# Performance work log

Hardware: AMD Instinct MI355X
Metric: run time of the kernel (lower is better)

## Reference

```python
import jax, jax.numpy as jnp
import numpy as np

BETA = 0.1
MARGIN = 0.1
LOSS_WEIGHT = 1.0
K = 4          # num_negative_samples_per_positive
EPS = 1e-6
C, D, P = 100000, 256, 65536


def _energy(p, c):
    """Euclidean entailment-cone energy: relu(apex_angle(p,c) - aperture(p))."""
    diff = c - p
    num = jnp.sum(c * c, -1) - jnp.sum(p * p, -1) - jnp.sum(diff * diff, -1)
    norm_p = jnp.linalg.norm(p, axis=-1)
    denom = 2.0 * norm_p * jnp.linalg.norm(diff, axis=-1) + EPS
    cosang = jnp.clip(num / denom, -1.0 + EPS, 1.0 - EPS)
    ang = jnp.arccos(cosang)
    aperture = jnp.arcsin(jnp.clip(BETA / (norm_p + EPS), 0.0, 1.0 - EPS))
    return jax.nn.relu(ang - aperture)


def setup_inputs() -> dict:
    key = jax.random.key(0)
    k1, k2, k3 = jax.random.split(key, 3)
    prototypes = jax.random.normal(k1, (C, D), dtype=jnp.float32)
    pairs = jax.random.randint(k2, (P, 2), 0, C, dtype=jnp.int32)
    neg_c = jax.random.randint(k3, (P * K,), 0, C, dtype=jnp.int32)
    return {"prototypes": prototypes, "pairs": pairs, "neg_c": neg_c}


def reference(prototypes, pairs, neg_c):
    # positive pairs: (parent, child) gathers
    p_pos = prototypes[pairs[:, 0]]                    # [P, D]
    c_pos = prototypes[pairs[:, 1]]                    # [P, D]
    avg_pos = _energy(p_pos, c_pos).mean()

    # negatives: each positive parent repeated K times vs sampled neg children
    neg_p_idx = jnp.repeat(pairs[:, 0], K)             # [P*K]
    p_neg = prototypes[neg_p_idx]                      # [P*K, D]
    c_neg = prototypes[neg_c]                          # [P*K, D]
    avg_neg = jax.nn.relu(MARGIN - _energy(p_neg, c_neg)).mean()

    return (avg_pos + avg_neg) * 0.5 * LOSS_WEIGHT
```

## Files before the change

kernel.cpp:

```cpp
#include <hip/hip_runtime.h>

#define BETA   0.1f
#define MARGIN 0.1f
#define EPSF   1e-6f
#define KNEG   4

__device__ __forceinline__ float gsum16(float v) {
    #pragma unroll
    for (int off = 8; off >= 1; off >>= 1)
        v += __shfl_xor(v, off, 64);
    return v;
}

__device__ __forceinline__ float wave_sum(float v) {
    #pragma unroll
    for (int off = 32; off >= 1; off >>= 1)
        v += __shfl_xor(v, off, 64);
    return v;
}

__device__ __forceinline__ float dot4(float4 a, float4 b) {
    return a.x*b.x + a.y*b.y + a.z*b.z + a.w*b.w;
}

__global__ __launch_bounds__(256) void cone_main(
    const float* __restrict__ proto,
    const int*   __restrict__ pairs,
    const int*   __restrict__ negc,
    float*       __restrict__ part,
    int P)
{
    const int lane = threadIdx.x & 63;
    const int wid  = threadIdx.x >> 6;
    const int sub  = lane >> 4;
    const int sl   = lane & 15;
    const int pair = (blockIdx.x * 4 + wid) * 4 + sub;

    float pos_e = 0.f, neg_e = 0.f;
    if (pair < P) {
        const int pi = pairs[2 * pair];
        int idx[5];
        idx[0] = pairs[2 * pair + 1];
        #pragma unroll
        for (int k = 0; k < KNEG; ++k) idx[1 + k] = negc[4 * pair + k];

        const float4* prow = (const float4*)(proto + (size_t)pi * 256);
        float4 pv[4];
        #pragma unroll
        for (int r = 0; r < 4; ++r) pv[r] = prow[sl + 16 * r];

        float4 cv[5][4];
        #pragma unroll
        for (int j = 0; j < 5; ++j) {
            const float4* crow = (const float4*)(proto + (size_t)idx[j] * 256);
            #pragma unroll
            for (int r = 0; r < 4; ++r) cv[j][r] = crow[sl + 16 * r];
        }

        float pp = 0.f;
        #pragma unroll
        for (int r = 0; r < 4; ++r) pp += dot4(pv[r], pv[r]);
        float p2     = gsum16(pp);
        float norm_p = sqrtf(p2);
        float apert  = asinf(fminf(fmaxf(BETA / (norm_p + EPSF), 0.f), 1.f - EPSF));

        #pragma unroll
        for (int j = 0; j < 5; ++j) {
            float cc = 0.f, dd = 0.f;
            #pragma unroll
            for (int r = 0; r < 4; ++r) {
                float4 c = cv[j][r], p = pv[r];
                cc += dot4(c, c);
                float dx = c.x - p.x, dy = c.y - p.y, dz = c.z - p.z, dw = c.w - p.w;
                dd += dx*dx + dy*dy + dz*dz + dw*dw;
            }
            float c2 = gsum16(cc);
            float d2 = gsum16(dd);
            float num    = c2 - p2 - d2;
            float denom  = 2.f * norm_p * sqrtf(d2) + EPSF;
            float cosang = fminf(fmaxf(num / denom, -1.f + EPSF), 1.f - EPSF);
            float e      = fmaxf(acosf(cosang) - apert, 0.f);
            if (j == 0) pos_e = e;
            else        neg_e += fmaxf(MARGIN - e, 0.f);
        }
    }

    __shared__ float sp[16], sn[16];
    if (sl == 0) { sp[wid * 4 + sub] = pos_e; sn[wid * 4 + sub] = neg_e; }
    __syncthreads();
    if (threadIdx.x == 0) {
        float ps = 0.f, ns = 0.f;
        #pragma unroll
        for (int i = 0; i < 16; ++i) { ps += sp[i]; ns += sn[i]; }
        part[2 * blockIdx.x]     = ps;
        part[2 * blockIdx.x + 1] = ns;
    }
}

__global__ __launch_bounds__(1024) void cone_final(
    const float* __restrict__ part, float* __restrict__ out, int nblocks, int P)
{
    float ps = 0.f, ns = 0.f;
    for (int i = threadIdx.x; i < nblocks; i += 1024) {
        ps += part[2 * i];
        ns += part[2 * i + 1];
    }
    ps = wave_sum(ps);
    ns = wave_sum(ns);
    const int lane = threadIdx.x & 63, wid = threadIdx.x >> 6;
    __shared__ float sp[16], sn[16];
    if (lane == 0) { sp[wid] = ps; sn[wid] = ns; }
    __syncthreads();
    if (threadIdx.x == 0) {
        float tp = 0.f, tn = 0.f;
        #pragma unroll
        for (int i = 0; i < 16; ++i) { tp += sp[i]; tn += sn[i]; }
        float fP = (float)P;
        out[0] = (tp / fP + tn / (fP * (float)KNEG)) * 0.5f;
    }
}

extern "C" void kernel_launch(void* const* d_in, const int* in_sizes, int n_in,
                              void* d_out, int out_size, void* d_ws, size_t ws_size,
                              hipStream_t stream) {
    const float* proto = (const float*)d_in[0];
    const int*   pairs = (const int*)d_in[1];
    const int*   negc  = (const int*)d_in[2];
    float*       part  = (float*)d_ws;
    const int P = in_sizes[1] / 2;
    const int nblocks = (P + 15) / 16;

    cone_main<<<nblocks, 256, 0, stream>>>(proto, pairs, negc, part, P);
    cone_final<<<1, 1024, 0, stream>>>(part, (float*)d_out, nblocks, P);
}
```

Before: 180.1 us.

## Stage gathered rows into LDS via direct global-to-LDS loads and batch transcendentals

Each block now handles 8 pairs. It gathers the parent, positive-child and four negative-child rows straight into shared memory with global_load_lds, where before each lane loaded them into registers. The dot products are reduced across 32-lane halves. The acos and asin calls are packed into one acos per lane, using asin = pi/2 - acos, so the transcendentals run across 12 lanes instead of being repeated by every lane. This trades register pressure and serial transcendental work for 48KB of LDS per block, which limits occupancy, and for twice as many blocks.

Measured after the change: 194.4 us. +7.9%, slower.

```diff
diff --git a/kernel.cpp b/kernel.cpp
--- a/kernel.cpp
+++ b/kernel.cpp
@@ -4,10 +4,17 @@
 #define MARGIN 0.1f
 #define EPSF   1e-6f
 #define KNEG   4
+#define PPB    8
+#define NROWS  (PPB * 6)
+#define PI_2   1.57079632679489662f
 
-__device__ __forceinline__ float gsum16(float v) {
+__device__ __forceinline__ float dot4(float4 a, float4 b) {
+    return a.x*b.x + a.y*b.y + a.z*b.z + a.w*b.w;
+}
+
+__device__ __forceinline__ float hsum32(float v) {
     #pragma unroll
-    for (int off = 8; off >= 1; off >>= 1)
+    for (int off = 16; off >= 1; off >>= 1)
         v += __shfl_xor(v, off, 64);
     return v;
 }
@@ -19,10 +26,6 @@
     return v;
 }
 
-__device__ __forceinline__ float dot4(float4 a, float4 b) {
-    return a.x*b.x + a.y*b.y + a.z*b.z + a.w*b.w;
-}
-
 __global__ __launch_bounds__(256) void cone_main(
     const float* __restrict__ proto,
     const int*   __restrict__ pairs,
@@ -30,70 +33,95 @@
     float*       __restrict__ part,
     int P)
 {
+    __shared__ float rows[NROWS * 256];
+    __shared__ float sp[4], sn[4];
+
     const int lane = threadIdx.x & 63;
-    const int wid  = threadIdx.x >> 6;
-    const int sub  = lane >> 4;
-    const int sl   = lane & 15;
-    const int pair = (blockIdx.x * 4 + wid) * 4 + sub;
+    const int w    = threadIdx.x >> 6;
+    const int blk  = blockIdx.x;
 
-    float pos_e = 0.f, neg_e = 0.f;
-    if (pair < P) {
-        const int pi = pairs[2 * pair];
-        int idx[5];
-        idx[0] = pairs[2 * pair + 1];
-        #pragma unroll
-        for (int k = 0; k < KNEG; ++k) idx[1 + k] = negc[4 * pair + k];
-
-        const float4* prow = (const float4*)(proto + (size_t)pi * 256);
-        float4 pv[4];
-        #pragma unroll
-        for (int r = 0; r < 4; ++r) pv[r] = prow[sl + 16 * r];
-
-        float4 cv[5][4];
-        #pragma unroll
-        for (int j = 0; j < 5; ++j) {
-            const float4* crow = (const float4*)(proto + (size_t)idx[j] * 256);
-            #pragma unroll
-            for (int r = 0; r < 4; ++r) cv[j][r] = crow[sl + 16 * r];
-        }
-
-        float pp = 0.f;
-        #pragma unroll
-        for (int r = 0; r < 4; ++r) pp += dot4(pv[r], pv[r]);
-        float p2     = gsum16(pp);
-        float norm_p = sqrtf(p2);
-        float apert  = asinf(fminf(fmaxf(BETA / (norm_p + EPSF), 0.f), 1.f - EPSF));
-
-        #pragma unroll
-        for (int j = 0; j < 5; ++j) {
-            float cc = 0.f, dd = 0.f;
-            #pragma unroll
-            for (int r = 0; r < 4; ++r) {
-                float4 c = cv[j][r], p = pv[r];
-                cc += dot4(c, c);
-                float dx = c.x - p.x, dy = c.y - p.y, dz = c.z - p.z, dw = c.w - p.w;
-                dd += dx*dx + dy*dy + dz*dz + dw*dw;
-            }
-            float c2 = gsum16(cc);
-            float d2 = gsum16(dd);
-            float num    = c2 - p2 - d2;
-            float denom  = 2.f * norm_p * sqrtf(d2) + EPSF;
-            float cosang = fminf(fmaxf(num / denom, -1.f + EPSF), 1.f - EPSF);
-            float e      = fmaxf(acosf(cosang) - apert, 0.f);
-            if (j == 0) pos_e = e;
-            else        neg_e += fmaxf(MARGIN - e, 0.f);
-        }
+    int myidx = 0;
+    {
+        int o1 = blk * (2 * PPB) + lane;
+        int o2 = blk * (4 * PPB) + (lane - 16);
+        if (lane < 16)      myidx = pairs[min(o1, 2 * P - 1)];
+        else if (lane < 48) myidx = negc[min(o2, 4 * P - 1)];
     }
 
-    __shared__ float sp[16], sn[16];
-    if (sl == 0) { sp[wid * 4 + sub] = pos_e; sn[wid * 4 + sub] = neg_e; }
+    #pragma unroll
+    for (int rr = 0; rr < 12; ++rr) {
+        const int r = w * 12 + rr;
+        const int q = r / 6, t = r % 6;
+        const int src = (t < 2) ? (2 * q + t) : (16 + 4 * q + (t - 2));
+        const int idx = __shfl(myidx, src, 64);
+        const float* gp = proto + (size_t)idx * 256 + lane * 4;
+        __builtin_amdgcn_global_load_lds(
+            (const __attribute__((address_space(1))) void*)gp,
+            (__attribute__((address_space(3))) void*)&rows[r * 256],
+            16, 0, 0);
+    }
+    __syncthreads();
+
+    const int q  = lane >> 5;
+    const int hl = lane & 31;
+    const int pl = w * 2 + q;
+    const float4* r4 = (const float4*)rows;
+
+    const int pbase = (pl * 6) * 64;
+    float4 p0 = r4[pbase + hl];
+    float4 p1 = r4[pbase + 32 + hl];
+    float p2 = hsum32(dot4(p0, p0) + dot4(p1, p1));
+    float norm_p = sqrtf(p2);
+    float asin_arg = fminf(fmaxf(BETA / (norm_p + EPSF), 0.f), 1.f - EPSF);
+
+    const int tq = (lane < 6) ? 0 : 1;
+    const int tj = lane - 6 * tq;
+    float my_t = 0.f;
+
+    #pragma unroll
+    for (int j = 1; j <= 5; ++j) {
+        const int cb = (pl * 6 + j) * 64;
+        float4 c0 = r4[cb + hl];
+        float4 c1 = r4[cb + 32 + hl];
+        float cc = dot4(c0, c0) + dot4(c1, c1);
+        float d0x = c0.x - p0.x, d0y = c0.y - p0.y, d0z = c0.z - p0.z, d0w = c0.w - p0.w;
+        float d1x = c1.x - p1.x, d1y = c1.y - p1.y, d1z = c1.z - p1.z, d1w = c1.w - p1.w;
+        float dd = d0x*d0x + d0y*d0y + d0z*d0z + d0w*d0w
+                 + d1x*d1x + d1y*d1y + d1z*d1z + d1w*d1w;
+        cc = hsum32(cc);
+        dd = hsum32(dd);
+        float num    = cc - p2 - dd;
+        float den    = 2.f * norm_p * sqrtf(dd) + EPSF;
+        float ca     = fminf(fmaxf(num / den, -1.f + EPSF), 1.f - EPSF);
+        float v0 = __shfl(ca, 0, 64);
+        float v1 = __shfl(ca, 32, 64);
+        my_t = (tj == j - 1) ? (tq ? v1 : v0) : my_t;
+    }
+    {
+        float v0 = __shfl(asin_arg, 0, 64);
+        float v1 = __shfl(asin_arg, 32, 64);
+        my_t = (tj == 5) ? (tq ? v1 : v0) : my_t;
+    }
+
+    float ang = acosf(my_t);
+
+    float a0 = __shfl(ang, 5, 64);
+    float a1 = __shfl(ang, 11, 64);
+    float apert = PI_2 - (tq ? a1 : a0);
+    float e = fmaxf(ang - apert, 0.f);
+
+    const int pair_g = blk * PPB + tq + 2 * w;
+    const bool valid = (lane < 12) && (pair_g < P);
+    float pos_c = (valid && tj == 0)            ? e                        : 0.f;
+    float neg_c = (valid && tj >= 1 && tj <= 5 - 1) ? fmaxf(MARGIN - e, 0.f) : 0.f;
+
+    float ps = wave_sum(pos_c);
+    float ns = wave_sum(neg_c);
+    if (lane == 0) { sp[w] = ps; sn[w] = ns; }
     __syncthreads();
     if (threadIdx.x == 0) {
-        float ps = 0.f, ns = 0.f;
-        #pragma unroll
-        for (int i = 0; i < 16; ++i) { ps += sp[i]; ns += sn[i]; }
-        part[2 * blockIdx.x]     = ps;
-        part[2 * blockIdx.x + 1] = ns;
+        part[2 * blk]     = sp[0] + sp[1] + sp[2] + sp[3];
+        part[2 * blk + 1] = sn[0] + sn[1] + sn[2] + sn[3];
     }
 }
 
@@ -128,7 +156,7 @@
     const int*   negc  = (const int*)d_in[2];
     float*       part  = (float*)d_ws;
     const int P = in_sizes[1] / 2;
-    const int nblocks = (P + 15) / 16;
+    const int nblocks = (P + PPB - 1) / PPB;
 
     cone_main<<<nblocks, 256, 0, stream>>>(proto, pairs, negc, part, P);
     cone_final<<<1, 1024, 0, stream>>>(part, (float*)d_out, nblocks, P);
```

## Convert prototype table to FP8 and gather compressed rows in main kernel

Applied to the files above, without the earlier changes.

Adds a pre-pass that quantizes the whole prototype table to FP8 in workspace. The main kernel then gathers 16-byte FP8 row slices instead of 64-byte FP32 slices and unpacks them with hardware conversion builtins, cutting random-gather traffic by about four times. The cost is an extra full-table conversion pass on every call, which reads 100 MB and writes 25 MB, plus a significant loss of precision in the norms and angles. The FP32 fallback path also now loads child rows inside the compute loop instead of prefetching all of them up front.

New measurement: 177.2 us. About the same (-1.6%).

```diff
diff --git a/kernel.cpp b/kernel.cpp
--- a/kernel.cpp
+++ b/kernel.cpp
@@ -5,25 +5,114 @@
 #define EPSF   1e-6f
 #define KNEG   4
 
+typedef float f2_t __attribute__((ext_vector_type(2)));
+
 __device__ __forceinline__ float gsum16(float v) {
     #pragma unroll
-    for (int off = 8; off >= 1; off >>= 1)
-        v += __shfl_xor(v, off, 64);
+    for (int off = 8; off >= 1; off >>= 1) v += __shfl_xor(v, off, 64);
     return v;
 }
-
 __device__ __forceinline__ float wave_sum(float v) {
     #pragma unroll
-    for (int off = 32; off >= 1; off >>= 1)
-        v += __shfl_xor(v, off, 64);
+    for (int off = 32; off >= 1; off >>= 1) v += __shfl_xor(v, off, 64);
     return v;
 }
-
 __device__ __forceinline__ float dot4(float4 a, float4 b) {
     return a.x*b.x + a.y*b.y + a.z*b.z + a.w*b.w;
 }
-
-__global__ __launch_bounds__(256) void cone_main(
+__device__ __forceinline__ void unpack4(unsigned int u, float* f) {
+    f2_t a = __builtin_amdgcn_cvt_pk_f32_fp8(u, false);
+    f[0] = a.x; f[1] = a.y;
+    a = __builtin_amdgcn_cvt_pk_f32_fp8(u, true);
+    f[2] = a.x; f[3] = a.y;
+}
+
+__global__ __launch_bounds__(256) void cvt_fp8(
+    const float* __restrict__ in, unsigned int* __restrict__ out, int n4)
+{
+    int i = blockIdx.x * 256 + threadIdx.x;
+    const int stride = gridDim.x * 256;
+    const float4* in4 = (const float4*)in;
+    for (; i < n4; i += stride) {
+        float4 v = in4[i];
+        unsigned int p = __builtin_amdgcn_cvt_pk_fp8_f32(v.x, v.y, 0u, false);
+        p = __builtin_amdgcn_cvt_pk_fp8_f32(v.z, v.w, p, true);
+        out[i] = p;
+    }
+}
+
+__global__ __launch_bounds__(256) void cone_main_fp8(
+    const uint4* __restrict__ tab,
+    const int*   __restrict__ pairs,
+    const int*   __restrict__ negc,
+    float*       __restrict__ part,
+    int P)
+{
+    const int lane = threadIdx.x & 63;
+    const int wid  = threadIdx.x >> 6;
+    const int sub  = lane >> 4;
+    const int sl   = lane & 15;
+    const int pair = (blockIdx.x * 4 + wid) * 4 + sub;
+
+    float pos_e = 0.f, neg_e = 0.f;
+    if (pair < P) {
+        const int pi = pairs[2 * pair];
+        int idx[5];
+        idx[0] = pairs[2 * pair + 1];
+        #pragma unroll
+        for (int k = 0; k < KNEG; ++k) idx[1 + k] = negc[4 * pair + k];
+
+        uint4 pu = tab[(size_t)pi * 16 + sl];
+        uint4 cu[5];
+        #pragma unroll
+        for (int j = 0; j < 5; ++j) cu[j] = tab[(size_t)idx[j] * 16 + sl];
+
+        float pf[16];
+        unpack4(pu.x, pf + 0);  unpack4(pu.y, pf + 4);
+        unpack4(pu.z, pf + 8);  unpack4(pu.w, pf + 12);
+        float pp = 0.f;
+        #pragma unroll
+        for (int d = 0; d < 16; ++d) pp += pf[d] * pf[d];
+        float p2     = gsum16(pp);
+        float norm_p = sqrtf(p2);
+        float apert  = asinf(fminf(fmaxf(BETA / (norm_p + EPSF), 0.f), 1.f - EPSF));
+
+        #pragma unroll
+        for (int j = 0; j < 5; ++j) {
+            float cf[16];
+            unpack4(cu[j].x, cf + 0);  unpack4(cu[j].y, cf + 4);
+            unpack4(cu[j].z, cf + 8);  unpack4(cu[j].w, cf + 12);
+            float cc = 0.f, dd = 0.f;
+            #pragma unroll
+            for (int d = 0; d < 16; ++d) {
+                cc += cf[d] * cf[d];
+                float t = cf[d] - pf[d];
+                dd += t * t;
+            }
+            float c2 = gsum16(cc);
+            float d2 = gsum16(dd);
+            float num    = c2 - p2 - d2;
+            float den    = 2.f * norm_p * sqrtf(d2) + EPSF;
+            float cosang = fminf(fmaxf(num / den, -1.f + EPSF), 1.f - EPSF);
+            float e      = fmaxf(acosf(cosang) - apert, 0.f);
+            if (j == 0) pos_e = e;
+            else        neg_e += fmaxf(MARGIN - e, 0.f);
+        }
+    }
+
+    __shared__ float sp[16], sn[16];
+    if (sl == 0) { sp[wid * 4 + sub] = pos_e; sn[wid * 4 + sub] = neg_e; }
+    __syncthreads();
+    if (threadIdx.x == 0) {
+        float ps = 0.f, ns = 0.f;
+        #pragma unroll
+        for (int i = 0; i < 16; ++i) { ps += sp[i]; ns += sn[i]; }
+        part[2 * blockIdx.x]     = ps;
+        part[2 * blockIdx.x + 1] = ns;
+    }
+}
+
+__global__ __launch_bounds__(256) void cone_main_f32(
     const float* __restrict__ proto,
     const int*   __restrict__ pairs,
     const int*   __restrict__ negc,
@@ -49,14 +138,6 @@
         #pragma unroll
         for (int r = 0; r < 4; ++r) pv[r] = prow[sl + 16 * r];
 
-        float4 cv[5][4];
-        #pragma unroll
-        for (int j = 0; j < 5; ++j) {
-            const float4* crow = (const float4*)(proto + (size_t)idx[j] * 256);
-            #pragma unroll
-            for (int r = 0; r < 4; ++r) cv[j][r] = crow[sl + 16 * r];
-        }
-
         float pp = 0.f;
         #pragma unroll
         for (int r = 0; r < 4; ++r) pp += dot4(pv[r], pv[r]);
@@ -66,10 +147,11 @@
 
         #pragma unroll
         for (int j = 0; j < 5; ++j) {
+            const float4* crow = (const float4*)(proto + (size_t)idx[j] * 256);
             float cc = 0.f, dd = 0.f;
             #pragma unroll
             for (int r = 0; r < 4; ++r) {
-                float4 c = cv[j][r], p = pv[r];
+                float4 c = crow[sl + 16 * r], p = pv[r];
                 cc += dot4(c, c);
                 float dx = c.x - p.x, dy = c.y - p.y, dz = c.z - p.z, dw = c.w - p.w;
                 dd += dx*dx + dy*dy + dz*dz + dw*dw;
@@ -77,8 +159,8 @@
             float c2 = gsum16(cc);
             float d2 = gsum16(dd);
             float num    = c2 - p2 - d2;
-            float denom  = 2.f * norm_p * sqrtf(d2) + EPSF;
-            float cosang = fminf(fmaxf(num / denom, -1.f + EPSF), 1.f - EPSF);
+            float den    = 2.f * norm_p * sqrtf(d2) + EPSF;
+            float cosang = fminf(fmaxf(num / den, -1.f + EPSF), 1.f - EPSF);
             float e      = fmaxf(acosf(cosang) - apert, 0.f);
             if (j == 0) pos_e = e;
             else        neg_e += fmaxf(MARGIN - e, 0.f);
@@ -126,10 +208,22 @@
     const float* proto = (const float*)d_in[0];
     const int*   pairs = (const int*)d_in[1];
     const int*   negc  = (const int*)d_in[2];
-    float*       part  = (float*)d_ws;
     const int P = in_sizes[1] / 2;
     const int nblocks = (P + 15) / 16;
 
-    cone_main<<<nblocks, 256, 0, stream>>>(proto, pairs, negc, part, P);
-    cone_final<<<1, 1024, 0, stream>>>(part, (float*)d_out, nblocks, P);
-}
+    const size_t tab_bytes = (size_t)in_sizes[0];
+    const size_t need = tab_bytes + (size_t)nblocks * 2 * sizeof(float);
+
+    if (ws_size >= need) {
+        unsigned int* tab  = (unsigned int*)d_ws;
+        float*        part = (float*)((char*)d_ws + tab_bytes);
+        const int n4 = in_sizes[0] / 4;
+        cvt_fp8<<<8192, 256, 0, stream>>>(proto, tab, n4);
+        cone_main_fp8<<<nblocks, 256, 0, stream>>>((const uint4*)tab, pairs, negc, part, P);
+        cone_final<<<1, 1024, 0, stream>>>(part, (float*)d_out, nblocks, P);
+    } else {
+        float* part = (float*)d_ws;
+        cone_main_f32<<<nblocks, 256, 0, stream>>>(proto, pairs, negc, part, P);
+        cone_final<<<1, 1024, 0, stream>>>(part, (float*)d_out, nblocks, P);
+    }
+}
```
